# Performance work log

Measured on AMD Instinct MI355X. Metric: run time of the kernel, lower is better.

Reference implementation:

```python
import jax, jax.numpy as jnp
import numpy as np

N_NODES = 100000
N_EDGES = 600000
N_GRAPHS = 64
BN_EPS = 1e-5


def setup_inputs() -> dict:
    key = jax.random.key(0)
    ks = jax.random.split(key, 32)
    inp = {
        "x": jax.random.normal(ks[0], (N_NODES, 128), dtype=jnp.float32),
        "edge_index": jax.random.randint(ks[1], (2, N_EDGES), 0, N_NODES, dtype=jnp.int64),
        "batch": jnp.sort(jax.random.randint(ks[2], (N_NODES,), 0, N_GRAPHS, dtype=jnp.int64)),
    }
    dims = [(128, 64, 64), (64, 64, 64), (64, 64, 96)]  # (in, hid, out) per GIN layer
    ki = 3
    for i, (d_in, d_hid, d_out) in enumerate(dims):
        inp[f"l{i}_w1"] = jax.random.normal(ks[ki], (d_in, d_hid), dtype=jnp.float32) * 0.05; ki += 1
        inp[f"l{i}_b1"] = jnp.zeros((d_hid,), dtype=jnp.float32)
        inp[f"l{i}_w2"] = jax.random.normal(ks[ki], (d_hid, d_out), dtype=jnp.float32) * 0.05; ki += 1
        inp[f"l{i}_b2"] = jnp.zeros((d_out,), dtype=jnp.float32)
        inp[f"bn{i}_g"] = jax.random.uniform(ks[ki], (d_out,), minval=0.5, maxval=1.5, dtype=jnp.float32); ki += 1
        inp[f"bn{i}_b"] = jax.random.normal(ks[ki], (d_out,), dtype=jnp.float32) * 0.05; ki += 1
        inp[f"bn{i}_m"] = jax.random.normal(ks[ki], (d_out,), dtype=jnp.float32) * 0.05; ki += 1
        inp[f"bn{i}_v"] = jax.random.uniform(ks[ki], (d_out,), minval=0.5, maxval=1.5, dtype=jnp.float32); ki += 1
    return inp


def _gin_layer(x, src, dst, w1, b1, w2, b2, g, bb, m, v):
    # GINConv (eps=0): h_i = MLP(x_i + sum_{j: j->i} x_j)
    aggr = jax.ops.segment_sum(x[src], dst, num_segments=N_NODES)
    h = x + aggr
    h = jax.nn.relu(h @ w1 + b1) @ w2 + b2
    # eval-mode BatchNorm1d + ReLU
    h = (h - m) * jax.lax.rsqrt(v + BN_EPS) * g + bb
    return jax.nn.relu(h)


def reference(x, edge_index, batch,
              l0_w1, l0_b1, l0_w2, l0_b2, bn0_g, bn0_b, bn0_m, bn0_v,
              l1_w1, l1_b1, l1_w2, l1_b2, bn1_g, bn1_b, bn1_m, bn1_v,
              l2_w1, l2_b1, l2_w2, l2_b2, bn2_g, bn2_b, bn2_m, bn2_v):
    src, dst = edge_index[0], edge_index[1]
    h = _gin_layer(x, src, dst, l0_w1, l0_b1, l0_w2, l0_b2, bn0_g, bn0_b, bn0_m, bn0_v)
    h = _gin_layer(h, src, dst, l1_w1, l1_b1, l1_w2, l1_b2, bn1_g, bn1_b, bn1_m, bn1_v)
    h = _gin_layer(h, src, dst, l2_w1, l2_b1, l2_w2, l2_b2, bn2_g, bn2_b, bn2_m, bn2_v)
    # global mean pool over graphs
    sums = jax.ops.segment_sum(h, batch, num_segments=N_GRAPHS)
    counts = jax.ops.segment_sum(jnp.ones((h.shape[0],), dtype=h.dtype), batch, num_segments=N_GRAPHS)
    return sums / jnp.maximum(counts, 1.0)[:, None]
```

## Files before the change

### kernel.cpp

```cpp
#include <hip/hip_runtime.h>

#define N_NODES 100000
#define N_GRAPHS 64
#define N_EDGES 600000
#define BN_EPS 1e-5f

typedef unsigned short bf16_t;

__device__ __forceinline__ unsigned short f2bf(float f) {
    unsigned int u = __float_as_uint(f);
    u += 0x7FFF + ((u >> 16) & 1);
    return (unsigned short)(u >> 16);
}
__device__ __forceinline__ float4 bf2f4(uint2 p) {
    float4 r;
    r.x = __uint_as_float(p.x << 16);
    r.y = __uint_as_float(p.x & 0xFFFF0000u);
    r.z = __uint_as_float(p.y << 16);
    r.w = __uint_as_float(p.y & 0xFFFF0000u);
    return r;
}
__device__ __forceinline__ uint2 pack4(float a, float b, float c, float d) {
    uint2 p;
    p.x = (unsigned)f2bf(a) | ((unsigned)f2bf(b) << 16);
    p.y = (unsigned)f2bf(c) | ((unsigned)f2bf(d) << 16);
    return p;
}

__global__ void deg_hist_kernel(const int* __restrict__ dst,
                                int* __restrict__ deg, int n_edges) {
    int e = blockIdx.x * blockDim.x + threadIdx.x;
    if (e < n_edges) atomicAdd(&deg[dst[e]], 1);
}

__global__ void scan1_kernel(const int* __restrict__ deg, int* __restrict__ excl,
                             int* __restrict__ partials, int n) {
    __shared__ int s[1024];
    int i = blockIdx.x * 1024 + threadIdx.x;
    int v = (i < n) ? deg[i] : 0;
    s[threadIdx.x] = v;
    __syncthreads();
    for (int off = 1; off < 1024; off <<= 1) {
        int t = (threadIdx.x >= (unsigned)off) ? s[threadIdx.x - off] : 0;
        __syncthreads();
        s[threadIdx.x] += t;
        __syncthreads();
    }
    if (i < n) excl[i] = s[threadIdx.x] - v;
    if (threadIdx.x == 1023) partials[blockIdx.x] = s[1023];
}

__global__ void scan2_kernel(int* partials, int nb) {
    __shared__ int s[128];
    int t = threadIdx.x;
    int v = (t < nb) ? partials[t] : 0;
    s[t] = v;
    __syncthreads();
    for (int off = 1; off < 128; off <<= 1) {
        int u = (t >= off) ? s[t - off] : 0;
        __syncthreads();
        s[t] += u;
        __syncthreads();
    }
    if (t < nb) partials[t] = s[t] - v;
}

__global__ void scan3_kernel(int* __restrict__ rowptr, const int* __restrict__ partials,
                             int n, int total) {
    int i = blockIdx.x * blockDim.x + threadIdx.x;
    if (i < n) rowptr[i] += partials[i >> 10];
    else if (i == n) rowptr[n] = total;
}

__global__ void fill_bounds_kernel(const int* __restrict__ src, const int* __restrict__ dst,
                                   const int* __restrict__ rowptr, int* __restrict__ cursor,
                                   int* __restrict__ eids, const int* __restrict__ batch,
                                   int* __restrict__ gstart, int n_edges, int n_nodes) {
    int e = blockIdx.x * blockDim.x + threadIdx.x;
    if (e < n_edges) {
        int t = dst[e];
        int pos = rowptr[t] + atomicAdd(&cursor[t], 1);
        eids[pos] = src[e];
    }
    if (e < n_nodes) {
        if (e == 0) {
            for (int g = 0; g <= batch[0]; ++g) gstart[g] = 0;
        } else {
            int b0 = batch[e - 1], b1 = batch[e];
            for (int g = b0 + 1; g <= b1; ++g) gstart[g] = e;
        }
        if (e == n_nodes - 1) {
            for (int g = batch[e] + 1; g <= N_GRAPHS; ++g) gstart[g] = n_nodes;
        }
    }
}

struct LayerPrep {
    const float *w1, *w2, *b2, *g, *bb, *m, *v;
    float *w1T, *w2sT, *bias2;
    int DIN, DOUT;
};
struct PrepAll { LayerPrep l[3]; };

__global__ void prep_all_kernel(PrepAll pa) {
    LayerPrep P = pa.l[blockIdx.y];
    int i = blockIdx.x * blockDim.x + threadIdx.x;
    if (i < 64 * P.DIN) {
        int j = i / P.DIN, k = i % P.DIN;
        P.w1T[i] = P.w1[k * 64 + j];
    }
    int i2 = i - 64 * P.DIN;
    if (i2 >= 0 && i2 < P.DOUT * 64) {
        int c = i2 / 64, j = i2 % 64;
        float s = P.g[c] * rsqrtf(P.v[c] + BN_EPS);
        P.w2sT[i2] = P.w2[j * P.DOUT + c] * s;
    }
    int i3 = i2 - P.DOUT * 64;
    if (i3 >= 0 && i3 < P.DOUT) {
        float s = P.g[i3] * rsqrtf(P.v[i3] + BN_EPS);
        P.bias2[i3] = (P.b2[i3] - P.m[i3]) * s + P.bb[i3];
    }
}

__global__ __launch_bounds__(256)
void pre_gemm_kernel(const float* __restrict__ x, const float* __restrict__ w1T,
                     bf16_t* __restrict__ y, int n_nodes) {
    __shared__ float w1s[64 * 128];
    const int tid = threadIdx.x;
    const long base = (long)blockIdx.x * 64;

    const float4* gw1 = (const float4*)w1T;
    for (int i4 = tid; i4 < 16 * 128; i4 += 256) {
        int row = i4 >> 5, k4 = i4 & 31;
        *(float4*)&w1s[row * 128 + ((k4 ^ ((row >> 2) & 7)) << 2)] = gw1[i4];
    }
    __syncthreads();

    const int jg = tid & 15, ng = tid >> 4, xw = jg & 7;
    const float* wp = &w1s[(jg * 4) * 128];
    const float4* xv = (const float4*)x;
    long r[4];
    #pragma unroll
    for (int i = 0; i < 4; ++i) {
        long rr = base + ng * 4 + i;
        r[i] = (rr < n_nodes) ? rr : (n_nodes - 1);
    }
    float acc[4][4] = {};
    #pragma unroll 4
    for (int k4 = 0; k4 < 32; ++k4) {
        const int ko = (k4 ^ xw) << 2;
        float4 w0 = *(const float4*)&wp[0 * 128 + ko];
        float4 w1v = *(const float4*)&wp[1 * 128 + ko];
        float4 w2v = *(const float4*)&wp[2 * 128 + ko];
        float4 w3v = *(const float4*)&wp[3 * 128 + ko];
        #pragma unroll
        for (int i = 0; i < 4; ++i) {
            float4 a = xv[r[i] * 32 + k4];
            acc[i][0] = fmaf(a.x, w0.x, fmaf(a.y, w0.y, fmaf(a.z, w0.z, fmaf(a.w, w0.w, acc[i][0]))));
            acc[i][1] = fmaf(a.x, w1v.x, fmaf(a.y, w1v.y, fmaf(a.z, w1v.z, fmaf(a.w, w1v.w, acc[i][1]))));
            acc[i][2] = fmaf(a.x, w2v.x, fmaf(a.y, w2v.y, fmaf(a.z, w2v.z, fmaf(a.w, w2v.w, acc[i][2]))));
            acc[i][3] = fmaf(a.x, w3v.x, fmaf(a.y, w3v.y, fmaf(a.z, w3v.z, fmaf(a.w, w3v.w, acc[i][3]))));
        }
    }
    #pragma unroll
    for (int i = 0; i < 4; ++i) {
        long n = base + ng * 4 + i;
        if (n < n_nodes) {
            *(uint2*)(y + n * 64 + jg * 4) = pack4(acc[i][0], acc[i][1], acc[i][2], acc[i][3]);
        }
    }
}

__global__ __launch_bounds__(256)
void gather64_kernel(const bf16_t* __restrict__ y, const int* __restrict__ rowptr,
                     const int* __restrict__ eids, const float* __restrict__ b1,
                     float* __restrict__ t, int n_nodes) {
    int node = blockIdx.x * 16 + (threadIdx.x >> 4);
    if (node >= n_nodes) return;
    int f4 = threadIdx.x & 15;
    const uint2* yv = (const uint2*)y;
    float4 acc = bf2f4(yv[(long)node * 16 + f4]);
    int b = rowptr[node], e = rowptr[node + 1];
    int i = b;
    for (; i + 3 < e; i += 4) {
        int s0 = eids[i], s1 = eids[i + 1], s2 = eids[i + 2], s3 = eids[i + 3];
        uint2 q0 = yv[(long)s0 * 16 + f4];
        uint2 q1 = yv[(long)s1 * 16 + f4];
        uint2 q2 = yv[(long)s2 * 16 + f4];
        uint2 q3 = yv[(long)s3 * 16 + f4];
        float4 r0 = bf2f4(q0), r1 = bf2f4(q1), r2 = bf2f4(q2), r3 = bf2f4(q3);
        acc.x += (r0.x + r1.x) + (r2.x + r3.x);
        acc.y += (r0.y + r1.y) + (r2.y + r3.y);
        acc.z += (r0.z + r1.z) + (r2.z + r3.z);
        acc.w += (r0.w + r1.w) + (r2.w + r3.w);
    }
    for (; i < e; ++i) {
        int s = eids[i];
        float4 r = bf2f4(yv[(long)s * 16 + f4]);
        acc.x += r.x; acc.y += r.y; acc.z += r.z; acc.w += r.w;
    }
    float4 bv = ((const float4*)b1)[f4];
    float4 o;
    o.x = fmaxf(acc.x + bv.x, 0.0f);
    o.y = fmaxf(acc.y + bv.y, 0.0f);
    o.z = fmaxf(acc.z + bv.z, 0.0f);
    o.w = fmaxf(acc.w + bv.w, 0.0f);
    ((float4*)t)[(long)node * 16 + f4] = o;
}

__global__ __launch_bounds__(256)
void fused_mid_kernel(const float* __restrict__ t, const float* __restrict__ w2sT,
                      const float* __restrict__ bias2, const float* __restrict__ w1nT,
                      bf16_t* __restrict__ ynext, int n_nodes) {
    constexpr int SS = 68;
    __shared__ float sT[64 * SS];
    __shared__ float wbuf[64 * 64];
    const int tid = threadIdx.x;
    const long base = (long)blockIdx.x * 64;

    const float4* gw2 = (const float4*)w2sT;
    for (int i4 = tid; i4 < 16 * 64; i4 += 256) {
        int row = i4 >> 4, k4 = i4 & 15;
        *(float4*)&wbuf[row * 64 + ((k4 ^ ((row >> 2) & 7)) << 2)] = gw2[i4];
    }
    __syncthreads();

    const int jg = tid & 15, ng = tid >> 4, xw = jg & 7;
    const float4* tv = (const float4*)(t + base * 64);

    float h[4][4];
    {
        const float* wp = &wbuf[(jg * 4) * 64];
        float acc[4][4] = {};
        #pragma unroll 4
        for (int k4 = 0; k4 < 16; ++k4) {
            const int ko = (k4 ^ xw) << 2;
            float4 w0 = *(const float4*)&wp[0 * 64 + ko];
            float4 w1v = *(const float4*)&wp[1 * 64 + ko];
            float4 w2v = *(const float4*)&wp[2 * 64 + ko];
            float4 w3v = *(const float4*)&wp[3 * 64 + ko];
            #pragma unroll
            for (int i = 0; i < 4; ++i) {
                float4 a = tv[(ng * 4 + i) * 16 + k4];
                acc[i][0] = fmaf(a.x, w0.x, fmaf(a.y, w0.y, fmaf(a.z, w0.z, fmaf(a.w, w0.w, acc[i][0]))));
                acc[i][1] = fmaf(a.x, w1v.x, fmaf(a.y, w1v.y, fmaf(a.z, w1v.z, fmaf(a.w, w1v.w, acc[i][1]))));
                acc[i][2] = fmaf(a.x, w2v.x, fmaf(a.y, w2v.y, fmaf(a.z, w2v.z, fmaf(a.w, w2v.w, acc[i][2]))));
                acc[i][3] = fmaf(a.x, w3v.x, fmaf(a.y, w3v.y, fmaf(a.z, w3v.z, fmaf(a.w, w3v.w, acc[i][3]))));
            }
        }
        float4 bv = *(const float4*)&bias2[jg * 4];
        #pragma unroll
        for (int i = 0; i < 4; ++i) {
            h[i][0] = fmaxf(acc[i][0] + bv.x, 0.0f);
            h[i][1] = fmaxf(acc[i][1] + bv.y, 0.0f);
            h[i][2] = fmaxf(acc[i][2] + bv.z, 0.0f);
            h[i][3] = fmaxf(acc[i][3] + bv.w, 0.0f);
        }
    }
    __syncthreads();

    #pragma unroll
    for (int i = 0; i < 4; ++i) {
        float4 hv = {h[i][0], h[i][1], h[i][2], h[i][3]};
        *(float4*)&sT[(ng * 4 + i) * SS + jg * 4] = hv;
    }
    const float4* gw1n = (const float4*)w1nT;
    for (int i4 = tid; i4 < 16 * 64; i4 += 256) {
        int row = i4 >> 4, k4 = i4 & 15;
        *(float4*)&wbuf[row * 64 + ((k4 ^ ((row >> 2) & 7)) << 2)] = gw1n[i4];
    }
    __syncthreads();

    {
        const float* ap = &sT[(ng * 4) * SS];
        const float* wp = &wbuf[(jg * 4) * 64];
        float acc[4][4] = {};
        #pragma unroll 4
        for (int k4 = 0; k4 < 16; ++k4) {
            const int ko = (k4 ^ xw) << 2;
            float4 w0 = *(const float4*)&wp[0 * 64 + ko];
            float4 w1v = *(const float4*)&wp[1 * 64 + ko];
            float4 w2v = *(const float4*)&wp[2 * 64 + ko];
            float4 w3v = *(const float4*)&wp[3 * 64 + ko];
            #pragma unroll
            for (int i = 0; i < 4; ++i) {
                float4 a = *(const float4*)&ap[i * SS + k4 * 4];
                acc[i][0] = fmaf(a.x, w0.x, fmaf(a.y, w0.y, fmaf(a.z, w0.z, fmaf(a.w, w0.w, acc[i][0]))));
                acc[i][1] = fmaf(a.x, w1v.x, fmaf(a.y, w1v.y, fmaf(a.z, w1v.z, fmaf(a.w, w1v.w, acc[i][1]))));
                acc[i][2] = fmaf(a.x, w2v.x, fmaf(a.y, w2v.y, fmaf(a.z, w2v.z, fmaf(a.w, w2v.w, acc[i][2]))));
                acc[i][3] = fmaf(a.x, w3v.x, fmaf(a.y, w3v.y, fmaf(a.z, w3v.z, fmaf(a.w, w3v.w, acc[i][3]))));
            }
        }
        #pragma unroll
        for (int i = 0; i < 4; ++i) {
            long n = base + ng * 4 + i;
            if (n < n_nodes) {
                *(uint2*)(ynext + n * 64 + jg * 4) = pack4(acc[i][0], acc[i][1], acc[i][2], acc[i][3]);
            }
        }
    }
}

__global__ __launch_bounds__(256)
void fused_final_kernel(const float* __restrict__ t, const float* __restrict__ w2sT,
                        const float* __restrict__ bias2, float* __restrict__ out,
                        int n_nodes) {
    constexpr int CPT = 6;
    __shared__ float w2s[96 * 64];
    const int tid = threadIdx.x;
    const long base = (long)blockIdx.x * 64;

    const float4* gw2 = (const float4*)w2sT;
    for (int i4 = tid; i4 < 96 * 16; i4 += 256) {
        int row = i4 >> 4, k4 = i4 & 15;
        *(float4*)&w2s[row * 64 + ((k4 ^ ((row / CPT) & 7)) << 2)] = gw2[i4];
    }
    __syncthreads();

    const int cg = tid & 15, ng = tid >> 4, xw = cg & 7;
    const float4* tv = (const float4*)(t + base * 64);
    const float* wp = &w2s[(cg * CPT) * 64];
    float acc[4][CPT] = {};
    #pragma unroll 4
    for (int k4 = 0; k4 < 16; ++k4) {
        const int ko = (k4 ^ xw) << 2;
        float4 wv[CPT];
        #pragma unroll
        for (int c = 0; c < CPT; ++c) wv[c] = *(const float4*)&wp[c * 64 + ko];
        #pragma unroll
        for (int i = 0; i < 4; ++i) {
            float4 h = tv[(ng * 4 + i) * 16 + k4];
            #pragma unroll
            for (int c = 0; c < CPT; ++c)
                acc[i][c] = fmaf(h.x, wv[c].x, fmaf(h.y, wv[c].y, fmaf(h.z, wv[c].z, fmaf(h.w, wv[c].w, acc[i][c]))));
        }
    }
    float bv[CPT];
    #pragma unroll
    for (int c = 0; c < CPT; ++c) bv[c] = bias2[cg * CPT + c];
    #pragma unroll
    for (int i = 0; i < 4; ++i) {
        long n = base + ng * 4 + i;
        if (n < n_nodes) {
            float* op = out + n * 96 + cg * CPT;
            #pragma unroll
            for (int c = 0; c < CPT; ++c) op[c] = fmaxf(acc[i][c] + bv[c], 0.0f);
        }
    }
}

#define POOL_SPLIT 16
__global__ __launch_bounds__(192)
void pool_seg_kernel(const float* __restrict__ h, const int* __restrict__ gstart,
                     float* __restrict__ part) {
    int g = blockIdx.x >> 4;
    int s = blockIdx.x & 15;
    int lo = gstart[g], hi = gstart[g + 1];
    int len = hi - lo;
    int seg = (len + POOL_SPLIT - 1) / POOL_SPLIT;
    int a = lo + s * seg;
    int b = a + seg; if (b > hi) b = hi;

    int f4 = threadIdx.x % 24;
    int chain = threadIdx.x / 24;
    const float4* hv = (const float4*)h;
    float4 acc = {0.0f, 0.0f, 0.0f, 0.0f};
    for (int n = a + chain; n < b; n += 8) {
        float4 v = hv[(long)n * 24 + f4];
        acc.x += v.x; acc.y += v.y; acc.z += v.z; acc.w += v.w;
    }
    __shared__ float4 red[8][24];
    red[chain][f4] = acc;
    __syncthreads();
    if (threadIdx.x < 24) {
        float4 t = red[0][threadIdx.x];
        #pragma unroll
        for (int c = 1; c < 8; ++c) {
            float4 r = red[c][threadIdx.x];
            t.x += r.x; t.y += r.y; t.z += r.z; t.w += r.w;
        }
        *(float4*)&part[((long)blockIdx.x) * 96 + threadIdx.x * 4] = t;
    }
}

__global__ void finalize_kernel(const float* __restrict__ part,
                                const int* __restrict__ gstart,
                                float* __restrict__ out) {
    int i = blockIdx.x * blockDim.x + threadIdx.x;
    if (i >= N_GRAPHS * 96) return;
    int g = i / 96, c = i - g * 96;
    float s = 0.0f;
    #pragma unroll
    for (int k = 0; k < POOL_SPLIT; ++k) s += part[((long)g * POOL_SPLIT + k) * 96 + c];
    float cnt = (float)(gstart[g + 1] - gstart[g]);
    out[i] = s / fmaxf(cnt, 1.0f);
}

static inline int cdiv_l(long a, int b) { return (int)((a + b - 1) / b); }

extern "C" void kernel_launch(void* const* d_in, const int* in_sizes, int n_in,
                              void* d_out, int out_size, void* d_ws, size_t ws_size,
                              hipStream_t stream) {
    const float* x     = (const float*)d_in[0];
    const int*   ei    = (const int*)d_in[1];
    const int*   src   = ei;
    const int*   dst   = ei + N_EDGES;
    const int*   batch = (const int*)d_in[2];

    const float* P[3][8];
    int p = 3;
    for (int l = 0; l < 3; ++l)
        for (int q = 0; q < 8; ++q)
            P[l][q] = (const float*)d_in[p++];

    const long NP = N_NODES + 64;
    char* wsb   = (char*)d_ws;
    bf16_t* yA  = (bf16_t*)wsb;
    bf16_t* yB  = yA + NP * 64;
    float* gB   = (float*)(yB + NP * 64);
    float* h2   = gB + NP * 64;
    float* q    = h2 + NP * 96;
    float* w1T[3], *w2sT[3], *bias2[3];
    for (int l = 0; l < 3; ++l) {
        w1T[l] = q;   q += 64 * 128;
        w2sT[l] = q;  q += 96 * 64;
        bias2[l] = q; q += 96;
    }
    float* part   = q;
    int* gstart   = (int*)(part + N_GRAPHS * POOL_SPLIT * 96);
    int* deg      = gstart + 72;
    int* cursor   = deg + N_NODES;
    int* partials = cursor + N_NODES;
    int* rowptr   = partials + 128;
    int* eids     = rowptr + (N_NODES + 1);

    const int B = 256;
    const int DIN[3]  = {128, 64, 64};
    const int DOUT[3] = {64, 64, 96};

    PrepAll pa;
    for (int l = 0; l < 3; ++l) {
        pa.l[l].w1 = P[l][0]; pa.l[l].w2 = P[l][2]; pa.l[l].b2 = P[l][3];
        pa.l[l].g = P[l][4];  pa.l[l].bb = P[l][5]; pa.l[l].m = P[l][6];
        pa.l[l].v = P[l][7];
        pa.l[l].w1T = w1T[l]; pa.l[l].w2sT = w2sT[l]; pa.l[l].bias2 = bias2[l];
        pa.l[l].DIN = DIN[l]; pa.l[l].DOUT = DOUT[l];
    }
    dim3 pgrid(cdiv_l(64 * 128 + 96 * 64 + 96, B), 3);
    prep_all_kernel<<<pgrid, B, 0, stream>>>(pa);

    hipMemsetAsync(deg, 0, (size_t)(2 * N_NODES + 128) * sizeof(int), stream);
    deg_hist_kernel<<<cdiv_l(N_EDGES, B), B, 0, stream>>>(dst, deg, N_EDGES);
    int nblk = cdiv_l(N_NODES, 1024);
    scan1_kernel<<<nblk, 1024, 0, stream>>>(deg, rowptr, partials, N_NODES);
    scan2_kernel<<<1, 128, 0, stream>>>(partials, nblk);
    scan3_kernel<<<cdiv_l(N_NODES + 1, B), B, 0, stream>>>(rowptr, partials, N_NODES, N_EDGES);
    fill_bounds_kernel<<<cdiv_l(N_EDGES, B), B, 0, stream>>>(
        src, dst, rowptr, cursor, eids, batch, gstart, N_EDGES, N_NODES);

    const int ntiles = cdiv_l(N_NODES, 64);
    const int ngather = cdiv_l(N_NODES, 16);

    pre_gemm_kernel<<<ntiles, 256, 0, stream>>>(x, w1T[0], yA, N_NODES);
    gather64_kernel<<<ngather, 256, 0, stream>>>(yA, rowptr, eids, P[0][1], gB, N_NODES);
    fused_mid_kernel<<<ntiles, 256, 0, stream>>>(
        gB, w2sT[0], bias2[0], w1T[1], yB, N_NODES);
    gather64_kernel<<<ngather, 256, 0, stream>>>(yB, rowptr, eids, P[1][1], gB, N_NODES);
    fused_mid_kernel<<<ntiles, 256, 0, stream>>>(
        gB, w2sT[1], bias2[1], w1T[2], yA, N_NODES);
    gather64_kernel<<<ngather, 256, 0, stream>>>(yA, rowptr, eids, P[2][1], gB, N_NODES);
    fused_final_kernel<<<ntiles, 256, 0, stream>>>(
        gB, w2sT[2], bias2[2], h2, N_NODES);

    pool_seg_kernel<<<N_GRAPHS * POOL_SPLIT, 192, 0, stream>>>(h2, gstart, part);
    finalize_kernel<<<cdiv_l(N_GRAPHS * 96, B), B, 0, stream>>>(
        part, gstart, (float*)d_out);
}
```

Measured before the change: 395.1 us.

## Merge CSR build and weight prep into one cooperative kernel, atomic pool finalize

```diff
diff --git a/kernel.cpp b/kernel.cpp
--- a/kernel.cpp
+++ b/kernel.cpp
@@ -1,4 +1,7 @@
 #include <hip/hip_runtime.h>
+#include <hip/hip_cooperative_groups.h>
+
+namespace cg = cooperative_groups;
 
 #define N_NODES 100000
 #define N_GRAPHS 64
@@ -27,74 +30,6 @@
     return p;
 }
 
-__global__ void deg_hist_kernel(const int* __restrict__ dst,
-                                int* __restrict__ deg, int n_edges) {
-    int e = blockIdx.x * blockDim.x + threadIdx.x;
-    if (e < n_edges) atomicAdd(&deg[dst[e]], 1);
-}
-
-__global__ void scan1_kernel(const int* __restrict__ deg, int* __restrict__ excl,
-                             int* __restrict__ partials, int n) {
-    __shared__ int s[1024];
-    int i = blockIdx.x * 1024 + threadIdx.x;
-    int v = (i < n) ? deg[i] : 0;
-    s[threadIdx.x] = v;
-    __syncthreads();
-    for (int off = 1; off < 1024; off <<= 1) {
-        int t = (threadIdx.x >= (unsigned)off) ? s[threadIdx.x - off] : 0;
-        __syncthreads();
-        s[threadIdx.x] += t;
-        __syncthreads();
-    }
-    if (i < n) excl[i] = s[threadIdx.x] - v;
-    if (threadIdx.x == 1023) partials[blockIdx.x] = s[1023];
-}
-
-__global__ void scan2_kernel(int* partials, int nb) {
-    __shared__ int s[128];
-    int t = threadIdx.x;
-    int v = (t < nb) ? partials[t] : 0;
-    s[t] = v;
-    __syncthreads();
-    for (int off = 1; off < 128; off <<= 1) {
-        int u = (t >= off) ? s[t - off] : 0;
-        __syncthreads();
-        s[t] += u;
-        __syncthreads();
-    }
-    if (t < nb) partials[t] = s[t] - v;
-}
-
-__global__ void scan3_kernel(int* __restrict__ rowptr, const int* __restrict__ partials,
-                             int n, int total) {
-    int i = blockIdx.x * blockDim.x + threadIdx.x;
-    if (i < n) rowptr[i] += partials[i >> 10];
-    else if (i == n) rowptr[n] = total;
-}
-
-__global__ void fill_bounds_kernel(const int* __restrict__ src, const int* __restrict__ dst,
-                                   const int* __restrict__ rowptr, int* __restrict__ cursor,
-                                   int* __restrict__ eids, const int* __restrict__ batch,
-                                   int* __restrict__ gstart, int n_edges, int n_nodes) {
-    int e = blockIdx.x * blockDim.x + threadIdx.x;
-    if (e < n_edges) {
-        int t = dst[e];
-        int pos = rowptr[t] + atomicAdd(&cursor[t], 1);
-        eids[pos] = src[e];
-    }
-    if (e < n_nodes) {
-        if (e == 0) {
-            for (int g = 0; g <= batch[0]; ++g) gstart[g] = 0;
-        } else {
-            int b0 = batch[e - 1], b1 = batch[e];
-            for (int g = b0 + 1; g <= b1; ++g) gstart[g] = e;
-        }
-        if (e == n_nodes - 1) {
-            for (int g = batch[e] + 1; g <= N_GRAPHS; ++g) gstart[g] = n_nodes;
-        }
-    }
-}
-
 struct LayerPrep {
     const float *w1, *w2, *b2, *g, *bb, *m, *v;
     float *w1T, *w2sT, *bias2;
@@ -102,23 +37,95 @@
 };
 struct PrepAll { LayerPrep l[3]; };
 
-__global__ void prep_all_kernel(PrepAll pa) {
-    LayerPrep P = pa.l[blockIdx.y];
-    int i = blockIdx.x * blockDim.x + threadIdx.x;
-    if (i < 64 * P.DIN) {
-        int j = i / P.DIN, k = i % P.DIN;
-        P.w1T[i] = P.w1[k * 64 + j];
-    }
-    int i2 = i - 64 * P.DIN;
-    if (i2 >= 0 && i2 < P.DOUT * 64) {
-        int c = i2 / 64, j = i2 % 64;
-        float s = P.g[c] * rsqrtf(P.v[c] + BN_EPS);
-        P.w2sT[i2] = P.w2[j * P.DOUT + c] * s;
-    }
-    int i3 = i2 - P.DOUT * 64;
-    if (i3 >= 0 && i3 < P.DOUT) {
-        float s = P.g[i3] * rsqrtf(P.v[i3] + BN_EPS);
-        P.bias2[i3] = (P.b2[i3] - P.m[i3]) * s + P.bb[i3];
+__global__ void csr_coop_kernel(const int* __restrict__ src, const int* __restrict__ dst,
+                                const int* __restrict__ batch,
+                                int* __restrict__ deg, int* __restrict__ cursor,
+                                int* __restrict__ rowptr, int* __restrict__ partials,
+                                int* __restrict__ eids, int* __restrict__ gstart,
+                                PrepAll pa, float* __restrict__ out_zero) {
+    cg::grid_group grid = cg::this_grid();
+    __shared__ int s[1024];
+    const int tid = blockIdx.x * blockDim.x + threadIdx.x;
+    const int nthreads = gridDim.x * blockDim.x;
+
+    for (int i = tid; i < N_NODES; i += nthreads) { deg[i] = 0; cursor[i] = 0; }
+    for (int i = tid; i < N_GRAPHS * 96; i += nthreads) out_zero[i] = 0.0f;
+    for (int l = 0; l < 3; ++l) {
+        LayerPrep P = pa.l[l];
+        int tot = 64 * P.DIN + P.DOUT * 64 + P.DOUT;
+        for (int i = tid; i < tot; i += nthreads) {
+            if (i < 64 * P.DIN) {
+                int j = i / P.DIN, k = i % P.DIN;
+                P.w1T[i] = P.w1[k * 64 + j];
+            } else if (i < 64 * P.DIN + P.DOUT * 64) {
+                int i2 = i - 64 * P.DIN;
+                int c = i2 / 64, j = i2 % 64;
+                float sc = P.g[c] * rsqrtf(P.v[c] + BN_EPS);
+                P.w2sT[i2] = P.w2[j * P.DOUT + c] * sc;
+            } else {
+                int i3 = i - 64 * P.DIN - P.DOUT * 64;
+                float sc = P.g[i3] * rsqrtf(P.v[i3] + BN_EPS);
+                P.bias2[i3] = (P.b2[i3] - P.m[i3]) * sc + P.bb[i3];
+            }
+        }
+    }
+    grid.sync();
+
+    for (int e = tid; e < N_EDGES; e += nthreads) atomicAdd(&deg[dst[e]], 1);
+    grid.sync();
+
+    {
+        int v = (tid < N_NODES) ? deg[tid] : 0;
+        s[threadIdx.x] = v;
+        __syncthreads();
+        for (int off = 1; off < 1024; off <<= 1) {
+            int t = (threadIdx.x >= (unsigned)off) ? s[threadIdx.x - off] : 0;
+            __syncthreads();
+            s[threadIdx.x] += t;
+            __syncthreads();
+        }
+        if (tid < N_NODES) rowptr[tid] = s[threadIdx.x] - v;
+        if (threadIdx.x == 1023) partials[blockIdx.x] = s[1023];
+    }
+    grid.sync();
+
+    if (blockIdx.x == 0) {
+        int t = threadIdx.x;
+        int v2 = 0;
+        if (t < 128) {
+            v2 = (t < (int)gridDim.x) ? partials[t] : 0;
+            s[t] = v2;
+        }
+        __syncthreads();
+        for (int off = 1; off < 128; off <<= 1) {
+            int u = (t < 128 && t >= off) ? s[t - off] : 0;
+            __syncthreads();
+            if (t < 128) s[t] += u;
+            __syncthreads();
+        }
+        if (t < (int)gridDim.x) partials[t] = s[t] - v2;
+    }
+    grid.sync();
+
+    if (tid < N_NODES) rowptr[tid] += partials[blockIdx.x];
+    else if (tid == N_NODES) rowptr[N_NODES] = N_EDGES;
+    grid.sync();
+
+    for (int e = tid; e < N_EDGES; e += nthreads) {
+        int t = dst[e];
+        int pos = rowptr[t] + atomicAdd(&cursor[t], 1);
+        eids[pos] = src[e];
+    }
+    for (int n = tid; n < N_NODES; n += nthreads) {
+        if (n == 0) {
+            for (int g = 0; g <= batch[0]; ++g) gstart[g] = 0;
+        } else {
+            int b0 = batch[n - 1], b1 = batch[n];
+            for (int g = b0 + 1; g <= b1; ++g) gstart[g] = n;
+        }
+        if (n == N_NODES - 1) {
+            for (int g = batch[n] + 1; g <= N_GRAPHS; ++g) gstart[g] = N_NODES;
+        }
     }
 }
 
@@ -127,7 +134,7 @@
                      bf16_t* __restrict__ y, int n_nodes) {
     __shared__ float w1s[64 * 128];
     const int tid = threadIdx.x;
-    const long base = (long)blockIdx.x * 64;
+    const long base = (long)blockIdx.x * 128;
 
     const float4* gw1 = (const float4*)w1T;
     for (int i4 = tid; i4 < 16 * 128; i4 += 256) {
@@ -139,14 +146,14 @@
     const int jg = tid & 15, ng = tid >> 4, xw = jg & 7;
     const float* wp = &w1s[(jg * 4) * 128];
     const float4* xv = (const float4*)x;
-    long r[4];
+    long r[8];
     #pragma unroll
-    for (int i = 0; i < 4; ++i) {
-        long rr = base + ng * 4 + i;
+    for (int i = 0; i < 8; ++i) {
+        long rr = base + ng * 8 + i;
         r[i] = (rr < n_nodes) ? rr : (n_nodes - 1);
     }
-    float acc[4][4] = {};
-    #pragma unroll 4
+    float acc[8][4] = {};
+    #pragma unroll 2
     for (int k4 = 0; k4 < 32; ++k4) {
         const int ko = (k4 ^ xw) << 2;
         float4 w0 = *(const float4*)&wp[0 * 128 + ko];
@@ -154,7 +161,7 @@
         float4 w2v = *(const float4*)&wp[2 * 128 + ko];
         float4 w3v = *(const float4*)&wp[3 * 128 + ko];
         #pragma unroll
-        for (int i = 0; i < 4; ++i) {
+        for (int i = 0; i < 8; ++i) {
             float4 a = xv[r[i] * 32 + k4];
             acc[i][0] = fmaf(a.x, w0.x, fmaf(a.y, w0.y, fmaf(a.z, w0.z, fmaf(a.w, w0.w, acc[i][0]))));
             acc[i][1] = fmaf(a.x, w1v.x, fmaf(a.y, w1v.y, fmaf(a.z, w1v.z, fmaf(a.w, w1v.w, acc[i][1]))));
@@ -163,8 +170,8 @@
         }
     }
     #pragma unroll
-    for (int i = 0; i < 4; ++i) {
-        long n = base + ng * 4 + i;
+    for (int i = 0; i < 8; ++i) {
+        long n = base + ng * 8 + i;
         if (n < n_nodes) {
             *(uint2*)(y + n * 64 + jg * 4) = pack4(acc[i][0], acc[i][1], acc[i][2], acc[i][3]);
         }
@@ -317,9 +324,9 @@
     }
     __syncthreads();
 
-    const int cg = tid & 15, ng = tid >> 4, xw = cg & 7;
+    const int cg_ = tid & 15, ng = tid >> 4, xw = cg_ & 7;
     const float4* tv = (const float4*)(t + base * 64);
-    const float* wp = &w2s[(cg * CPT) * 64];
+    const float* wp = &w2s[(cg_ * CPT) * 64];
     float acc[4][CPT] = {};
     #pragma unroll 4
     for (int k4 = 0; k4 < 16; ++k4) {
@@ -337,12 +344,12 @@
     }
     float bv[CPT];
     #pragma unroll
-    for (int c = 0; c < CPT; ++c) bv[c] = bias2[cg * CPT + c];
+    for (int c = 0; c < CPT; ++c) bv[c] = bias2[cg_ * CPT + c];
     #pragma unroll
     for (int i = 0; i < 4; ++i) {
         long n = base + ng * 4 + i;
         if (n < n_nodes) {
-            float* op = out + n * 96 + cg * CPT;
+            float* op = out + n * 96 + cg_ * CPT;
             #pragma unroll
             for (int c = 0; c < CPT; ++c) op[c] = fmaxf(acc[i][c] + bv[c], 0.0f);
         }
@@ -352,7 +359,7 @@
 #define POOL_SPLIT 16
 __global__ __launch_bounds__(192)
 void pool_seg_kernel(const float* __restrict__ h, const int* __restrict__ gstart,
-                     float* __restrict__ part) {
+                     float* __restrict__ out) {
     int g = blockIdx.x >> 4;
     int s = blockIdx.x & 15;
     int lo = gstart[g], hi = gstart[g + 1];
@@ -379,21 +386,13 @@
             float4 r = red[c][threadIdx.x];
             t.x += r.x; t.y += r.y; t.z += r.z; t.w += r.w;
         }
-        *(float4*)&part[((long)blockIdx.x) * 96 + threadIdx.x * 4] = t;
-    }
-}
-
-__global__ void finalize_kernel(const float* __restrict__ part,
-                                const int* __restrict__ gstart,
-                                float* __restrict__ out) {
-    int i = blockIdx.x * blockDim.x + threadIdx.x;
-    if (i >= N_GRAPHS * 96) return;
-    int g = i / 96, c = i - g * 96;
-    float s = 0.0f;
-    #pragma unroll
-    for (int k = 0; k < POOL_SPLIT; ++k) s += part[((long)g * POOL_SPLIT + k) * 96 + c];
-    float cnt = (float)(gstart[g + 1] - gstart[g]);
-    out[i] = s / fmaxf(cnt, 1.0f);
+        float inv = 1.0f / fmaxf((float)len, 1.0f);
+        float* op = &out[g * 96 + threadIdx.x * 4];
+        atomicAdd(op + 0, t.x * inv);
+        atomicAdd(op + 1, t.y * inv);
+        atomicAdd(op + 2, t.z * inv);
+        atomicAdd(op + 3, t.w * inv);
+    }
 }
 
 static inline int cdiv_l(long a, int b) { return (int)((a + b - 1) / b); }
@@ -413,7 +412,7 @@
         for (int q = 0; q < 8; ++q)
             P[l][q] = (const float*)d_in[p++];
 
-    const long NP = N_NODES + 64;
+    const long NP = N_NODES + 128;
     char* wsb   = (char*)d_ws;
     bf16_t* yA  = (bf16_t*)wsb;
     bf16_t* yB  = yA + NP * 64;
@@ -426,15 +425,13 @@
         w2sT[l] = q;  q += 96 * 64;
         bias2[l] = q; q += 96;
     }
-    float* part   = q;
-    int* gstart   = (int*)(part + N_GRAPHS * POOL_SPLIT * 96);
+    int* gstart   = (int*)q;
     int* deg      = gstart + 72;
     int* cursor   = deg + N_NODES;
     int* partials = cursor + N_NODES;
     int* rowptr   = partials + 128;
     int* eids     = rowptr + (N_NODES + 1);
 
-    const int B = 256;
     const int DIN[3]  = {128, 64, 64};
     const int DOUT[3] = {64, 64, 96};
 
@@ -446,22 +443,18 @@
         pa.l[l].w1T = w1T[l]; pa.l[l].w2sT = w2sT[l]; pa.l[l].bias2 = bias2[l];
         pa.l[l].DIN = DIN[l]; pa.l[l].DOUT = DOUT[l];
     }
-    dim3 pgrid(cdiv_l(64 * 128 + 96 * 64 + 96, B), 3);
-    prep_all_kernel<<<pgrid, B, 0, stream>>>(pa);
-
-    hipMemsetAsync(deg, 0, (size_t)(2 * N_NODES + 128) * sizeof(int), stream);
-    deg_hist_kernel<<<cdiv_l(N_EDGES, B), B, 0, stream>>>(dst, deg, N_EDGES);
-    int nblk = cdiv_l(N_NODES, 1024);
-    scan1_kernel<<<nblk, 1024, 0, stream>>>(deg, rowptr, partials, N_NODES);
-    scan2_kernel<<<1, 128, 0, stream>>>(partials, nblk);
-    scan3_kernel<<<cdiv_l(N_NODES + 1, B), B, 0, stream>>>(rowptr, partials, N_NODES, N_EDGES);
-    fill_bounds_kernel<<<cdiv_l(N_EDGES, B), B, 0, stream>>>(
-        src, dst, rowptr, cursor, eids, batch, gstart, N_EDGES, N_NODES);
+
+    float* outp = (float*)d_out;
+    void* kargs[] = {(void*)&src, (void*)&dst, (void*)&batch, (void*)&deg,
+                     (void*)&cursor, (void*)&rowptr, (void*)&partials,
+                     (void*)&eids, (void*)&gstart, (void*)&pa, (void*)&outp};
+    hipLaunchCooperativeKernel((void*)csr_coop_kernel, dim3(98), dim3(1024),
+                               kargs, 0, stream);
 
     const int ntiles = cdiv_l(N_NODES, 64);
     const int ngather = cdiv_l(N_NODES, 16);
 
-    pre_gemm_kernel<<<ntiles, 256, 0, stream>>>(x, w1T[0], yA, N_NODES);
+    pre_gemm_kernel<<<cdiv_l(N_NODES, 128), 256, 0, stream>>>(x, w1T[0], yA, N_NODES);
     gather64_kernel<<<ngather, 256, 0, stream>>>(yA, rowptr, eids, P[0][1], gB, N_NODES);
     fused_mid_kernel<<<ntiles, 256, 0, stream>>>(
         gB, w2sT[0], bias2[0], w1T[1], yB, N_NODES);
@@ -472,7 +465,5 @@
     fused_final_kernel<<<ntiles, 256, 0, stream>>>(
         gB, w2sT[2], bias2[2], h2, N_NODES);
 
-    pool_seg_kernel<<<N_GRAPHS * POOL_SPLIT, 192, 0, stream>>>(h2, gstart, part);
-    finalize_kernel<<<cdiv_l(N_GRAPHS * 96, B), B, 0, stream>>>(
-        part, gstart, (float*)d_out);
-}
+    pool_seg_kernel<<<N_GRAPHS * POOL_SPLIT, 192, 0, stream>>>(h2, gstart, outp);
+}
```

Measured after the change: 490.1 us. 24.0% more time.

## Widen gather loads, fold memset into prep, pool directly with atomics

Applied to the files above, without the earlier changes.

```diff
diff --git a/kernel.cpp b/kernel.cpp
--- a/kernel.cpp
+++ b/kernel.cpp
@@ -25,6 +25,16 @@
     p.x = (unsigned)f2bf(a) | ((unsigned)f2bf(b) << 16);
     p.y = (unsigned)f2bf(c) | ((unsigned)f2bf(d) << 16);
     return p;
+}
+__device__ __forceinline__ void bf8_acc(uint4 q, float* acc) {
+    acc[0] += __uint_as_float(q.x << 16);
+    acc[1] += __uint_as_float(q.x & 0xFFFF0000u);
+    acc[2] += __uint_as_float(q.y << 16);
+    acc[3] += __uint_as_float(q.y & 0xFFFF0000u);
+    acc[4] += __uint_as_float(q.z << 16);
+    acc[5] += __uint_as_float(q.z & 0xFFFF0000u);
+    acc[6] += __uint_as_float(q.w << 16);
+    acc[7] += __uint_as_float(q.w & 0xFFFF0000u);
 }
 
 __global__ void deg_hist_kernel(const int* __restrict__ dst,
@@ -102,9 +112,15 @@
 };
 struct PrepAll { LayerPrep l[3]; };
 
-__global__ void prep_all_kernel(PrepAll pa) {
+__global__ void prep_all_kernel(PrepAll pa, int* __restrict__ deg,
+                                int* __restrict__ cursor, float* __restrict__ out_zero) {
     LayerPrep P = pa.l[blockIdx.y];
     int i = blockIdx.x * blockDim.x + threadIdx.x;
+    if (blockIdx.y == 0) {
+        int stride = gridDim.x * blockDim.x;
+        for (int k = i; k < N_NODES; k += stride) { deg[k] = 0; cursor[k] = 0; }
+        for (int k = i; k < N_GRAPHS * 96; k += stride) out_zero[k] = 0.0f;
+    }
     if (i < 64 * P.DIN) {
         int j = i / P.DIN, k = i % P.DIN;
         P.w1T[i] = P.w1[k * 64 + j];
@@ -175,37 +191,37 @@
 void gather64_kernel(const bf16_t* __restrict__ y, const int* __restrict__ rowptr,
                      const int* __restrict__ eids, const float* __restrict__ b1,
                      float* __restrict__ t, int n_nodes) {
-    int node = blockIdx.x * 16 + (threadIdx.x >> 4);
+    int node = blockIdx.x * 32 + (threadIdx.x >> 3);
     if (node >= n_nodes) return;
-    int f4 = threadIdx.x & 15;
-    const uint2* yv = (const uint2*)y;
-    float4 acc = bf2f4(yv[(long)node * 16 + f4]);
+    int f = threadIdx.x & 7;
+    const uint4* yv = (const uint4*)y;
+    float acc[8] = {};
+    bf8_acc(yv[(long)node * 8 + f], acc);
     int b = rowptr[node], e = rowptr[node + 1];
     int i = b;
     for (; i + 3 < e; i += 4) {
         int s0 = eids[i], s1 = eids[i + 1], s2 = eids[i + 2], s3 = eids[i + 3];
-        uint2 q0 = yv[(long)s0 * 16 + f4];
-        uint2 q1 = yv[(long)s1 * 16 + f4];
-        uint2 q2 = yv[(long)s2 * 16 + f4];
-        uint2 q3 = yv[(long)s3 * 16 + f4];
-        float4 r0 = bf2f4(q0), r1 = bf2f4(q1), r2 = bf2f4(q2), r3 = bf2f4(q3);
-        acc.x += (r0.x + r1.x) + (r2.x + r3.x);
-        acc.y += (r0.y + r1.y) + (r2.y + r3.y);
-        acc.z += (r0.z + r1.z) + (r2.z + r3.z);
-        acc.w += (r0.w + r1.w) + (r2.w + r3.w);
-    }
-    for (; i < e; ++i) {
-        int s = eids[i];
-        float4 r = bf2f4(yv[(long)s * 16 + f4]);
-        acc.x += r.x; acc.y += r.y; acc.z += r.z; acc.w += r.w;
-    }
-    float4 bv = ((const float4*)b1)[f4];
-    float4 o;
-    o.x = fmaxf(acc.x + bv.x, 0.0f);
-    o.y = fmaxf(acc.y + bv.y, 0.0f);
-    o.z = fmaxf(acc.z + bv.z, 0.0f);
-    o.w = fmaxf(acc.w + bv.w, 0.0f);
-    ((float4*)t)[(long)node * 16 + f4] = o;
+        uint4 q0 = yv[(long)s0 * 8 + f];
+        uint4 q1 = yv[(long)s1 * 8 + f];
+        uint4 q2 = yv[(long)s2 * 8 + f];
+        uint4 q3 = yv[(long)s3 * 8 + f];
+        bf8_acc(q0, acc); bf8_acc(q1, acc); bf8_acc(q2, acc); bf8_acc(q3, acc);
+    }
+    for (; i < e; ++i) bf8_acc(yv[(long)eids[i] * 8 + f], acc);
+
+    float4 b0 = ((const float4*)b1)[f * 2];
+    float4 b1v = ((const float4*)b1)[f * 2 + 1];
+    float4 o0, o1;
+    o0.x = fmaxf(acc[0] + b0.x, 0.0f);
+    o0.y = fmaxf(acc[1] + b0.y, 0.0f);
+    o0.z = fmaxf(acc[2] + b0.z, 0.0f);
+    o0.w = fmaxf(acc[3] + b0.w, 0.0f);
+    o1.x = fmaxf(acc[4] + b1v.x, 0.0f);
+    o1.y = fmaxf(acc[5] + b1v.y, 0.0f);
+    o1.z = fmaxf(acc[6] + b1v.z, 0.0f);
+    o1.w = fmaxf(acc[7] + b1v.w, 0.0f);
+    ((float4*)t)[(long)node * 16 + f * 2] = o0;
+    ((float4*)t)[(long)node * 16 + f * 2 + 1] = o1;
 }
 
 __global__ __launch_bounds__(256)
@@ -317,9 +333,9 @@
     }
     __syncthreads();
 
-    const int cg = tid & 15, ng = tid >> 4, xw = cg & 7;
+    const int cg_ = tid & 15, ng = tid >> 4, xw = cg_ & 7;
     const float4* tv = (const float4*)(t + base * 64);
-    const float* wp = &w2s[(cg * CPT) * 64];
+    const float* wp = &w2s[(cg_ * CPT) * 64];
     float acc[4][CPT] = {};
     #pragma unroll 4
     for (int k4 = 0; k4 < 16; ++k4) {
@@ -337,12 +353,12 @@
     }
     float bv[CPT];
     #pragma unroll
-    for (int c = 0; c < CPT; ++c) bv[c] = bias2[cg * CPT + c];
+    for (int c = 0; c < CPT; ++c) bv[c] = bias2[cg_ * CPT + c];
     #pragma unroll
     for (int i = 0; i < 4; ++i) {
         long n = base + ng * 4 + i;
         if (n < n_nodes) {
-            float* op = out + n * 96 + cg * CPT;
+            float* op = out + n * 96 + cg_ * CPT;
             #pragma unroll
             for (int c = 0; c < CPT; ++c) op[c] = fmaxf(acc[i][c] + bv[c], 0.0f);
         }
@@ -352,7 +368,7 @@
 #define POOL_SPLIT 16
 __global__ __launch_bounds__(192)
 void pool_seg_kernel(const float* __restrict__ h, const int* __restrict__ gstart,
-                     float* __restrict__ part) {
+                     float* __restrict__ out) {
     int g = blockIdx.x >> 4;
     int s = blockIdx.x & 15;
     int lo = gstart[g], hi = gstart[g + 1];
@@ -379,21 +395,13 @@
             float4 r = red[c][threadIdx.x];
             t.x += r.x; t.y += r.y; t.z += r.z; t.w += r.w;
         }
-        *(float4*)&part[((long)blockIdx.x) * 96 + threadIdx.x * 4] = t;
-    }
-}
-
-__global__ void finalize_kernel(const float* __restrict__ part,
-                                const int* __restrict__ gstart,
-                                float* __restrict__ out) {
-    int i = blockIdx.x * blockDim.x + threadIdx.x;
-    if (i >= N_GRAPHS * 96) return;
-    int g = i / 96, c = i - g * 96;
-    float s = 0.0f;
-    #pragma unroll
-    for (int k = 0; k < POOL_SPLIT; ++k) s += part[((long)g * POOL_SPLIT + k) * 96 + c];
-    float cnt = (float)(gstart[g + 1] - gstart[g]);
-    out[i] = s / fmaxf(cnt, 1.0f);
+        float inv = 1.0f / fmaxf((float)len, 1.0f);
+        float* op = &out[g * 96 + threadIdx.x * 4];
+        atomicAdd(op + 0, t.x * inv);
+        atomicAdd(op + 1, t.y * inv);
+        atomicAdd(op + 2, t.z * inv);
+        atomicAdd(op + 3, t.w * inv);
+    }
 }
 
 static inline int cdiv_l(long a, int b) { return (int)((a + b - 1) / b); }
@@ -413,7 +421,7 @@
         for (int q = 0; q < 8; ++q)
             P[l][q] = (const float*)d_in[p++];
 
-    const long NP = N_NODES + 64;
+    const long NP = N_NODES + 128;
     char* wsb   = (char*)d_ws;
     bf16_t* yA  = (bf16_t*)wsb;
     bf16_t* yB  = yA + NP * 64;
@@ -426,8 +434,7 @@
         w2sT[l] = q;  q += 96 * 64;
         bias2[l] = q; q += 96;
     }
-    float* part   = q;
-    int* gstart   = (int*)(part + N_GRAPHS * POOL_SPLIT * 96);
+    int* gstart   = (int*)q;
     int* deg      = gstart + 72;
     int* cursor   = deg + N_NODES;
     int* partials = cursor + N_NODES;
@@ -447,9 +454,8 @@
         pa.l[l].DIN = DIN[l]; pa.l[l].DOUT = DOUT[l];
     }
     dim3 pgrid(cdiv_l(64 * 128 + 96 * 64 + 96, B), 3);
-    prep_all_kernel<<<pgrid, B, 0, stream>>>(pa);
-
-    hipMemsetAsync(deg, 0, (size_t)(2 * N_NODES + 128) * sizeof(int), stream);
+    prep_all_kernel<<<pgrid, B, 0, stream>>>(pa, deg, cursor, (float*)d_out);
+
     deg_hist_kernel<<<cdiv_l(N_EDGES, B), B, 0, stream>>>(dst, deg, N_EDGES);
     int nblk = cdiv_l(N_NODES, 1024);
     scan1_kernel<<<nblk, 1024, 0, stream>>>(deg, rowptr, partials, N_NODES);
@@ -459,7 +465,7 @@
         src, dst, rowptr, cursor, eids, batch, gstart, N_EDGES, N_NODES);
 
     const int ntiles = cdiv_l(N_NODES, 64);
-    const int ngather = cdiv_l(N_NODES, 16);
+    const int ngather = cdiv_l(N_NODES, 32);
 
     pre_gemm_kernel<<<ntiles, 256, 0, stream>>>(x, w1T[0], yA, N_NODES);
     gather64_kernel<<<ngather, 256, 0, stream>>>(yA, rowptr, eids, P[0][1], gB, N_NODES);
@@ -472,7 +478,5 @@
     fused_final_kernel<<<ntiles, 256, 0, stream>>>(
         gB, w2sT[2], bias2[2], h2, N_NODES);
 
-    pool_seg_kernel<<<N_GRAPHS * POOL_SPLIT, 192, 0, stream>>>(h2, gstart, part);
-    finalize_kernel<<<cdiv_l(N_GRAPHS * 96, B), B, 0, stream>>>(
-        part, gstart, (float*)d_out);
-}
+    pool_seg_kernel<<<N_GRAPHS * POOL_SPLIT, 192, 0, stream>>>(h2, gstart, (float*)d_out);
+}
```

New measurement: 387.2 us. 1.02x faster.
